# Optimization experiments

Hardware: AMD Instinct MI355X
Metric: run time of the kernel (lower is better)

Reference implementation:

```python
import jax, jax.numpy as jnp
import numpy as np

# Module constants (from init_kwargs)
P = 10000          # query points
G = 6400           # gaussians
C = 18             # semantic classes
H, W, D = 200, 200, 16
GRID = 0.5
SCALE_MULT = 3.0
PC_MIN = jnp.array([-50.0, -50.0, -5.0], dtype=jnp.float32)
COV_IDX = np.array([0, 4, 8, 1, 5, 2])  # xx, yy, zz, xy, yz, xz of flattened 3x3


def setup_inputs() -> dict:
    key = jax.random.key(0)
    k1, k2, k3, k4, k5, k6 = jax.random.split(key, 6)
    extent = jnp.array([H, W, D], jnp.float32) * GRID  # [100, 100, 8] meters
    eps = 1e-3  # keep strictly inside grid so int voxel coords are in-range
    pts = PC_MIN + jax.random.uniform(k1, (1, P, 3), jnp.float32) * (extent - eps)
    means3D = PC_MIN + jax.random.uniform(k2, (1, G, 3), jnp.float32) * (extent - eps)
    opacities = jax.random.uniform(k3, (1, G), jnp.float32)
    semantics = jax.random.normal(k4, (1, G, C), jnp.float32)
    # scales in [0.2, 1.0] m -> radii = ceil(max_scale*3/0.5) >= 2 (assert radii >= 1)
    scales = 0.2 + 0.8 * jax.random.uniform(k5, (1, G, 3), jnp.float32)
    # cov3D is the (symmetric PD) precision matrix: R diag(1/s^2) R^T
    A = jax.random.normal(k6, (1, G, 3, 3), jnp.float32)
    Q, _ = jnp.linalg.qr(A)
    inv_var = 1.0 / (scales ** 2)
    cov3D = jnp.einsum('bgij,bgj,bgkj->bgik', Q, inv_var, Q)
    return dict(pts=pts, means3D=means3D, opacities=opacities,
                semantics=semantics, scales=scales, cov3D=cov3D)


def reference(pts, means3D, opacities, semantics, scales, cov3D):
    # squeeze batch dim (module asserts batch == 1)
    p = pts[0]                     # [P,3]
    mu = means3D[0]                # [G,3]
    op = opacities[0]              # [G]
    sem = semantics[0]             # [G,C]
    sc = scales[0]                 # [G,3]
    cov = cov3D[0].reshape(G, 9)[:, COV_IDX]  # [G,6]: xx,yy,zz,xy,yz,xz

    # integer voxel coords (cast truncates; coords are non-negative in-range)
    p_int = ((p - PC_MIN) / GRID).astype(jnp.int32)                              # [P,3]
    m_int = ((jax.lax.stop_gradient(mu) - PC_MIN) / GRID).astype(jnp.int32)      # [G,3]
    radii = jnp.ceil(sc.max(-1) * SCALE_MULT / GRID).astype(jnp.int32)           # [G]

    # voxel-box test: point voxel within per-axis radius of gaussian voxel
    mask = (jnp.abs(p_int[:, None, :] - m_int[None, :, :]) <= radii[None, :, None]).all(-1)  # [P,G]

    # Mahalanobis power with precision matrix entries
    d = p[:, None, :] - mu[None, :, :]           # [P,G,3]
    dx, dy, dz = d[..., 0], d[..., 1], d[..., 2]
    power = (-0.5 * (cov[None, :, 0] * dx * dx
                     + cov[None, :, 1] * dy * dy
                     + cov[None, :, 2] * dz * dz)
             - cov[None, :, 3] * dx * dy
             - cov[None, :, 4] * dy * dz
             - cov[None, :, 5] * dx * dz)        # [P,G]

    w = jnp.where(mask, jnp.exp(power) * op[None, :], 0.0)  # [P,G]
    logits = w @ sem                                         # [P,C]
    return logits
```

## Files before the change

kernel.cpp:

```cpp
#include <hip/hip_runtime.h>
#include <math.h>

#define P_TOTAL 10000
#define G_TOTAL 6400
#define C_CLS   18
#define CS_SH   3
#define NCX     25
#define NCELL   (NCX * NCX)
#define MAXE    256
#define NTHR    256


__global__ void la_pack(const float* __restrict__ means3D,
                        const float* __restrict__ scales,
                        int4* __restrict__ boxes,
                        int* __restrict__ counts) {
    int tid = blockIdx.x * NTHR + threadIdx.x;
    if (tid < G_TOTAL) {
        int g = tid;
        float mx = means3D[g * 3 + 0];
        float my = means3D[g * 3 + 1];
        float mz = means3D[g * 3 + 2];
        float sx = scales[g * 3 + 0];
        float sy = scales[g * 3 + 1];
        float sz = scales[g * 3 + 2];
        int mix = (int)((mx + 50.0f) * 2.0f);
        int miy = (int)((my + 50.0f) * 2.0f);
        int miz = (int)((mz + 5.0f) * 2.0f);
        int r = (int)ceilf((fmaxf(fmaxf(sx, sy), sz) * 3.0f) * 2.0f);
        int w = 2 * r;
        boxes[g] = make_int4(mix - r, miy - r, miz - r, (w << 16) | g);
    } else if (tid < G_TOTAL + NCELL) {
        counts[tid - G_TOTAL] = 0;
    }
}


__global__ void la_scat(const int4* __restrict__ boxes,
                        int* __restrict__ counts,
                        int4* __restrict__ entries) {
    int tid = blockIdx.x * NTHR + threadIdx.x;
    int g = tid >> 2;
    int j = tid & 3;
    int4 b = boxes[g];
    int w = b.w >> 16;
    int cx0 = max(b.x, 0) >> CS_SH;
    int cx1 = min(b.x + w, 199) >> CS_SH;
    int cy0 = max(b.y, 0) >> CS_SH;
    int cy1 = min(b.y + w, 199) >> CS_SH;
    int nx = cx1 - cx0 + 1;
    int ny = cy1 - cy0 + 1;
    for (int k = j; k < 9; k += 4) {
        int dx = k % 3, dy = k / 3;
        if (dx < nx && dy < ny) {
            int cell = (cy0 + dy) * NCX + (cx0 + dx);
            int slot = atomicAdd(&counts[cell], 1);
            if (slot < MAXE) entries[(size_t)cell * MAXE + slot] = b;
        }
    }
}


__global__ void __launch_bounds__(NTHR)
la_gather(const float* __restrict__ pts,
          const float* __restrict__ means3D,
          const float* __restrict__ opacities,
          const float* __restrict__ semantics,
          const float* __restrict__ cov3D,
          const int* __restrict__ counts,
          const int4* __restrict__ entries,
          float* __restrict__ out) {
    const int lane = threadIdx.x & 63;
    const int pt = blockIdx.x * 4 + (threadIdx.x >> 6);

    float px = pts[pt * 3 + 0];
    float py = pts[pt * 3 + 1];
    float pz = pts[pt * 3 + 2];
    int pix = (int)((px + 50.0f) * 2.0f);
    int piy = (int)((py + 50.0f) * 2.0f);
    int piz = (int)((pz + 5.0f) * 2.0f);

    int cell = (piy >> CS_SH) * NCX + (pix >> CS_SH);
    int cnt = min(counts[cell], MAXE);
    const int4* eb = entries + (size_t)cell * MAXE;

    float acc = 0.0f;

    for (int base = 0; base < cnt; base += 64) {
        int i = base + lane;
        float wgt = 0.0f;
        int gid = 0;
        if (i < cnt) {
            int4 b = eb[i];
            unsigned w  = ((unsigned)b.w) >> 16;
            unsigned ux = (unsigned)(pix - b.x);
            unsigned uy = (unsigned)(piy - b.y);
            unsigned uz = (unsigned)(piz - b.z);
            if (ux <= w && uy <= w && uz <= w) {
                gid = b.w & 0xffff;
                float mx = means3D[gid * 3 + 0];
                float my = means3D[gid * 3 + 1];
                float mz = means3D[gid * 3 + 2];
                const float* cv = cov3D + (size_t)gid * 9;
                float dx = px - mx, dy = py - my, dz = pz - mz;
                float pw = -0.5f * (cv[0] * dx * dx + cv[4] * dy * dy + cv[8] * dz * dz)
                           - cv[1] * dx * dy - cv[5] * dy * dz - cv[2] * dx * dz;
                wgt = __expf(pw) * opacities[gid];
            }
        }
        unsigned long long m = __ballot(wgt != 0.0f);
        while (m) {
            int h = (int)__builtin_ctzll(m);
            m &= m - 1;
            float wh = __shfl(wgt, h, 64);
            int   gh = __shfl(gid, h, 64);
            if (lane < C_CLS)
                acc = fmaf(wh, semantics[(size_t)gh * C_CLS + lane], acc);
        }
    }

    if (lane < C_CLS)
        out[(size_t)pt * C_CLS + lane] = acc;
}

extern "C" void kernel_launch(void* const* d_in, const int* in_sizes, int n_in,
                              void* d_out, int out_size, void* d_ws, size_t ws_size,
                              hipStream_t stream) {
    const float* pts      = (const float*)d_in[0];
    const float* means3D  = (const float*)d_in[1];
    const float* opac     = (const float*)d_in[2];
    const float* sem      = (const float*)d_in[3];
    const float* scales   = (const float*)d_in[4];
    const float* cov3D    = (const float*)d_in[5];
    float* out = (float*)d_out;

    char* ws = (char*)d_ws;
    int4* boxes   = (int4*)ws;
    int*  counts  = (int*)(ws + 102400);
    int4* entries = (int4*)(ws + 106496);

    la_pack<<<(G_TOTAL + NCELL + NTHR - 1) / NTHR, NTHR, 0, stream>>>(means3D, scales,
                                                                      boxes, counts);
    la_scat<<<(G_TOTAL * 4) / NTHR, NTHR, 0, stream>>>(boxes, counts, entries);
    la_gather<<<P_TOTAL / 4, NTHR, 0, stream>>>(pts, means3D, opac, sem, cov3D,
                                                counts, entries, out);
}
```

Measured before the change: 33.08 us.

## Fuse binning and gather into one per-cell kernel with shared-memory lists

Replaces the three-kernel pipeline (pack, scatter into global cell bins, gather per point) with a single kernel that runs one block per grid cell. Each block scans every point and every gaussian to build shared-memory lists of the points in its cell and the gaussians whose boxes overlap it, then evaluates those points against those gaussians. This removes two launches and the global atomic bin traffic. In exchange, every one of the 625 blocks re-reads all 10000 points and 6400 gaussians. The fixed per-cell point cap of 96 could silently drop points in denser cells.

New measurement: 31.02 us. 6.2% less time.

```diff
diff --git a/kernel.cpp b/kernel.cpp
--- a/kernel.cpp
+++ b/kernel.cpp
@@ -7,17 +7,42 @@
 #define CS_SH   3
 #define NCX     25
 #define NCELL   (NCX * NCX)
-#define MAXE    256
-#define NTHR    256
+#define BCAP    256
+#define PCAP    96
+#define NTHR    512
 
+__global__ void __launch_bounds__(NTHR)
+la_cell1(const float* __restrict__ pts,
+         const float* __restrict__ means3D,
+         const float* __restrict__ opacities,
+         const float* __restrict__ semantics,
+         const float* __restrict__ scales,
+         const float* __restrict__ cov3D,
+         float* __restrict__ out) {
+    __shared__ int4 sbox[BCAP];
+    __shared__ int  splist[PCAP];
+    __shared__ int  snb, snp;
 
-__global__ void la_pack(const float* __restrict__ means3D,
-                        const float* __restrict__ scales,
-                        int4* __restrict__ boxes,
-                        int* __restrict__ counts) {
-    int tid = blockIdx.x * NTHR + threadIdx.x;
-    if (tid < G_TOTAL) {
-        int g = tid;
+    const int t = threadIdx.x;
+    const int cell = blockIdx.x;
+    const int ccx = cell % NCX;
+    const int ccy = cell / NCX;
+
+    if (t == 0) { snb = 0; snp = 0; }
+    __syncthreads();
+
+    for (int i = t; i < P_TOTAL; i += NTHR) {
+        float px = pts[i * 3 + 0];
+        float py = pts[i * 3 + 1];
+        int cx = ((int)((px + 50.0f) * 2.0f)) >> CS_SH;
+        int cy = ((int)((py + 50.0f) * 2.0f)) >> CS_SH;
+        if (cx == ccx && cy == ccy) {
+            int s = atomicAdd(&snp, 1);
+            if (s < PCAP) splist[s] = i;
+        }
+    }
+
+    for (int g = t; g < G_TOTAL; g += NTHR) {
         float mx = means3D[g * 3 + 0];
         float my = means3D[g * 3 + 1];
         float mz = means3D[g * 3 + 2];
@@ -29,98 +54,68 @@
         int miz = (int)((mz + 5.0f) * 2.0f);
         int r = (int)ceilf((fmaxf(fmaxf(sx, sy), sz) * 3.0f) * 2.0f);
         int w = 2 * r;
-        boxes[g] = make_int4(mix - r, miy - r, miz - r, (w << 16) | g);
-    } else if (tid < G_TOTAL + NCELL) {
-        counts[tid - G_TOTAL] = 0;
-    }
-}
-
-
-__global__ void la_scat(const int4* __restrict__ boxes,
-                        int* __restrict__ counts,
-                        int4* __restrict__ entries) {
-    int tid = blockIdx.x * NTHR + threadIdx.x;
-    int g = tid >> 2;
-    int j = tid & 3;
-    int4 b = boxes[g];
-    int w = b.w >> 16;
-    int cx0 = max(b.x, 0) >> CS_SH;
-    int cx1 = min(b.x + w, 199) >> CS_SH;
-    int cy0 = max(b.y, 0) >> CS_SH;
-    int cy1 = min(b.y + w, 199) >> CS_SH;
-    int nx = cx1 - cx0 + 1;
-    int ny = cy1 - cy0 + 1;
-    for (int k = j; k < 9; k += 4) {
-        int dx = k % 3, dy = k / 3;
-        if (dx < nx && dy < ny) {
-            int cell = (cy0 + dy) * NCX + (cx0 + dx);
-            int slot = atomicAdd(&counts[cell], 1);
-            if (slot < MAXE) entries[(size_t)cell * MAXE + slot] = b;
+        int minx = mix - r, miny = miy - r, minz = miz - r;
+        int cx0 = max(minx, 0) >> CS_SH;
+        int cx1 = min(minx + w, 199) >> CS_SH;
+        int cy0 = max(miny, 0) >> CS_SH;
+        int cy1 = min(miny + w, 199) >> CS_SH;
+        if (ccx >= cx0 && ccx <= cx1 && ccy >= cy0 && ccy <= cy1) {
+            int s = atomicAdd(&snb, 1);
+            if (s < BCAP) sbox[s] = make_int4(minx, miny, minz, (w << 16) | g);
         }
     }
-}
+    __syncthreads();
 
+    const int np = min(snp, PCAP);
+    const int nb = min(snb, BCAP);
+    const int wv = t >> 6, lane = t & 63;
 
-__global__ void __launch_bounds__(NTHR)
-la_gather(const float* __restrict__ pts,
-          const float* __restrict__ means3D,
-          const float* __restrict__ opacities,
-          const float* __restrict__ semantics,
-          const float* __restrict__ cov3D,
-          const int* __restrict__ counts,
-          const int4* __restrict__ entries,
-          float* __restrict__ out) {
-    const int lane = threadIdx.x & 63;
-    const int pt = blockIdx.x * 4 + (threadIdx.x >> 6);
+    for (int idx = wv; idx < np; idx += NTHR / 64) {
+        int pt = splist[idx];
+        float px = pts[pt * 3 + 0];
+        float py = pts[pt * 3 + 1];
+        float pz = pts[pt * 3 + 2];
+        int pix = (int)((px + 50.0f) * 2.0f);
+        int piy = (int)((py + 50.0f) * 2.0f);
+        int piz = (int)((pz + 5.0f) * 2.0f);
 
-    float px = pts[pt * 3 + 0];
-    float py = pts[pt * 3 + 1];
-    float pz = pts[pt * 3 + 2];
-    int pix = (int)((px + 50.0f) * 2.0f);
-    int piy = (int)((py + 50.0f) * 2.0f);
-    int piz = (int)((pz + 5.0f) * 2.0f);
-
-    int cell = (piy >> CS_SH) * NCX + (pix >> CS_SH);
-    int cnt = min(counts[cell], MAXE);
-    const int4* eb = entries + (size_t)cell * MAXE;
-
-    float acc = 0.0f;
-
-    for (int base = 0; base < cnt; base += 64) {
-        int i = base + lane;
-        float wgt = 0.0f;
-        int gid = 0;
-        if (i < cnt) {
-            int4 b = eb[i];
-            unsigned w  = ((unsigned)b.w) >> 16;
-            unsigned ux = (unsigned)(pix - b.x);
-            unsigned uy = (unsigned)(piy - b.y);
-            unsigned uz = (unsigned)(piz - b.z);
-            if (ux <= w && uy <= w && uz <= w) {
-                gid = b.w & 0xffff;
-                float mx = means3D[gid * 3 + 0];
-                float my = means3D[gid * 3 + 1];
-                float mz = means3D[gid * 3 + 2];
-                const float* cv = cov3D + (size_t)gid * 9;
-                float dx = px - mx, dy = py - my, dz = pz - mz;
-                float pw = -0.5f * (cv[0] * dx * dx + cv[4] * dy * dy + cv[8] * dz * dz)
-                           - cv[1] * dx * dy - cv[5] * dy * dz - cv[2] * dx * dz;
-                wgt = __expf(pw) * opacities[gid];
+        float acc = 0.0f;
+        for (int base = 0; base < nb; base += 64) {
+            int i = base + lane;
+            float wgt = 0.0f;
+            int gid = 0;
+            if (i < nb) {
+                int4 b = sbox[i];
+                unsigned w  = ((unsigned)b.w) >> 16;
+                unsigned ux = (unsigned)(pix - b.x);
+                unsigned uy = (unsigned)(piy - b.y);
+                unsigned uz = (unsigned)(piz - b.z);
+                if (ux <= w && uy <= w && uz <= w) {
+                    gid = b.w & 0xffff;
+                    float mx = means3D[gid * 3 + 0];
+                    float my = means3D[gid * 3 + 1];
+                    float mz = means3D[gid * 3 + 2];
+                    const float* cv = cov3D + (size_t)gid * 9;
+                    float dx = px - mx, dy = py - my, dz = pz - mz;
+                    float pw = -0.5f * (cv[0] * dx * dx + cv[4] * dy * dy + cv[8] * dz * dz)
+                               - cv[1] * dx * dy - cv[5] * dy * dz - cv[2] * dx * dz;
+                    wgt = __expf(pw) * opacities[gid];
+                }
+            }
+            unsigned long long m = __ballot(wgt != 0.0f);
+            while (m) {
+                int h = (int)__builtin_ctzll(m);
+                m &= m - 1;
+                float wh = __shfl(wgt, h, 64);
+                int   gh = __shfl(gid, h, 64);
+                if (lane < C_CLS)
+                    acc = fmaf(wh, semantics[(size_t)gh * C_CLS + lane], acc);
             }
         }
-        unsigned long long m = __ballot(wgt != 0.0f);
-        while (m) {
-            int h = (int)__builtin_ctzll(m);
-            m &= m - 1;
-            float wh = __shfl(wgt, h, 64);
-            int   gh = __shfl(gid, h, 64);
-            if (lane < C_CLS)
-                acc = fmaf(wh, semantics[(size_t)gh * C_CLS + lane], acc);
-        }
+
+        if (lane < C_CLS)
+            out[(size_t)pt * C_CLS + lane] = acc;
     }
-
-    if (lane < C_CLS)
-        out[(size_t)pt * C_CLS + lane] = acc;
 }
 
 extern "C" void kernel_launch(void* const* d_in, const int* in_sizes, int n_in,
@@ -134,14 +129,5 @@
     const float* cov3D    = (const float*)d_in[5];
     float* out = (float*)d_out;
 
-    char* ws = (char*)d_ws;
-    int4* boxes   = (int4*)ws;
-    int*  counts  = (int*)(ws + 102400);
-    int4* entries = (int4*)(ws + 106496);
-
-    la_pack<<<(G_TOTAL + NCELL + NTHR - 1) / NTHR, NTHR, 0, stream>>>(means3D, scales,
-                                                                      boxes, counts);
-    la_scat<<<(G_TOTAL * 4) / NTHR, NTHR, 0, stream>>>(boxes, counts, entries);
-    la_gather<<<P_TOTAL / 4, NTHR, 0, stream>>>(pts, means3D, opac, sem, cov3D,
-                                                counts, entries, out);
+    la_cell1<<<NCELL, NTHR, 0, stream>>>(pts, means3D, opac, sem, scales, cov3D, out);
 }
```
